# Kernel tuning notes

Measured on AMD Instinct MI355X. Metric: run time of the kernel, lower is better.

## Reference

```python
import jax, jax.numpy as jnp
import numpy as np

NUM_VIEWS = 6
NUM_HEADS = 16
NUM_LAYERS = 2
DIST_THRESHOLD = 10.0
EPS = 1e-5


def layer_norm(x, g, b):
    m = jnp.mean(x, axis=-1, keepdims=True)
    v = jnp.mean((x - m) ** 2, axis=-1, keepdims=True)
    return (x - m) / jnp.sqrt(v + EPS) * g + b


def build_mask(coords3d, num_views, threshold):
    # coords3d: (B, T, 3) -> bool mask (B, T, T), True = masked
    B, T, _ = coords3d.shape
    tpv = T // num_views
    c = jnp.nan_to_num(coords3d, nan=0.0, posinf=100.0, neginf=-100.0)
    view_ids = jnp.repeat(jnp.arange(num_views), tpv)
    same_view = view_ids[:, None] == view_ids[None, :]  # (T, T)
    dist_sq = jnp.sum((c[:, :, None, :] - c[:, None, :, :]) ** 2, axis=-1)  # (B,T,T)
    mask = same_view[None] | (dist_sq > threshold * threshold)
    all_masked = jnp.all(mask, axis=-1)  # (B, T)
    eye = jnp.eye(T, dtype=bool)
    # unmask diagonal for rows that are fully masked (matches torch fix)
    mask = jnp.where(all_masked[:, :, None] & eye[None], False, mask)
    return mask


def mha(x, qkv_w, qkv_b, out_w, out_b, mask, num_heads):
    # x: (B,T,C); qkv_w: (3C,C); out_w: (C,C); mask: (B,T,T) True=masked
    B, T, C = x.shape
    hd = C // num_heads
    qkv = x @ qkv_w.T + qkv_b  # (B,T,3C)
    q, k, v = jnp.split(qkv, 3, axis=-1)
    def heads(t):
        return t.reshape(B, T, num_heads, hd).transpose(0, 2, 1, 3)  # (B,H,T,hd)
    q, k, v = heads(q), heads(k), heads(v)
    scale = 1.0 / jnp.sqrt(jnp.asarray(hd, x.dtype))
    scores = jnp.einsum('bhqd,bhkd->bhqk', q * scale, k)
    scores = jnp.where(mask[:, None], -jnp.inf, scores)
    attn = jax.nn.softmax(scores, axis=-1)
    o = jnp.einsum('bhqk,bhkd->bhqd', attn, v)  # (B,H,T,hd)
    o = o.transpose(0, 2, 1, 3).reshape(B, T, C)
    return o @ out_w.T + out_b


def setup_inputs() -> dict:
    key = jax.random.key(0)
    B, T, C, L = 2, 1536, 1024, NUM_LAYERS
    ks = jax.random.split(key, 16)
    s = 0.02
    inp = {
        'pos_embed': jax.random.normal(ks[0], (B, T, C), jnp.float32),
        'coords3d': jax.random.normal(ks[1], (B, T, 3), jnp.float32) * 8.0,
        'ln1_g': jnp.ones((L, C), jnp.float32),
        'ln1_b': jnp.zeros((L, C), jnp.float32),
        'qkv_w': jax.random.normal(ks[2], (L, 3 * C, C), jnp.float32) * s,
        'qkv_b': jnp.zeros((L, 3 * C), jnp.float32),
        'out_w': jax.random.normal(ks[3], (L, C, C), jnp.float32) * s,
        'out_b': jnp.zeros((L, C), jnp.float32),
        'ln2_g': jnp.ones((L, C), jnp.float32),
        'ln2_b': jnp.zeros((L, C), jnp.float32),
        'ffn_w1': jax.random.normal(ks[4], (L, 4 * C, C), jnp.float32) * s,
        'ffn_b1': jnp.zeros((L, 4 * C), jnp.float32),
        'ffn_w2': jax.random.normal(ks[5], (L, C, 4 * C), jnp.float32) * s,
        'ffn_b2': jnp.zeros((L, C), jnp.float32),
        'norm_g': jnp.ones((C,), jnp.float32),
        'norm_b': jnp.zeros((C,), jnp.float32),
    }
    return inp


def reference(pos_embed, coords3d, ln1_g, ln1_b, qkv_w, qkv_b, out_w, out_b,
              ln2_g, ln2_b, ffn_w1, ffn_b1, ffn_w2, ffn_b2, norm_g, norm_b):
    mask = build_mask(coords3d, NUM_VIEWS, DIST_THRESHOLD)
    x = pos_embed
    for l in range(NUM_LAYERS):
        xn = layer_norm(x, ln1_g[l], ln1_b[l])
        x = x + mha(xn, qkv_w[l], qkv_b[l], out_w[l], out_b[l], mask, NUM_HEADS)
        xn = layer_norm(x, ln2_g[l], ln2_b[l])
        h = jax.nn.gelu(xn @ ffn_w1[l].T + ffn_b1[l], approximate=False)
        x = x + (h @ ffn_w2[l].T + ffn_b2[l])
    return layer_norm(x, norm_g, norm_b)
```

## Files before the change

### kernel.cpp

```cpp
#include <hip/hip_runtime.h>

#define TT 1536
#define CC 1024
#define NH 16
#define HD 64
#define NL 2
#define NB 2
#define MM (NB*TT)

typedef unsigned short u16;
typedef unsigned int u32;
typedef unsigned long long u64;
typedef __attribute__((ext_vector_type(8))) short short8v;
typedef __attribute__((ext_vector_type(4))) float f32x4;

__device__ __forceinline__ u16 f2bf(float f){
  u32 u = __float_as_uint(f);
  u32 r = (u + 0x7FFFu + ((u >> 16) & 1u)) >> 16;
  return (u16)r;
}

__device__ __forceinline__ void gload_lds16(const void* g, void* l){
  __builtin_amdgcn_global_load_lds(
      (const __attribute__((address_space(1))) void*)g,
      (__attribute__((address_space(3))) void*)l, 16, 0, 0);
}

__device__ __forceinline__ f32x4 mfma16(short8v a, short8v b, f32x4 c){
  return __builtin_amdgcn_mfma_f32_16x16x32_bf16(a, b, c, 0, 0, 0);
}

__device__ __forceinline__ float exp2f_fast(float x){
  return __builtin_amdgcn_exp2f(x);
}

__device__ __forceinline__ u32 cvt_pk_bf16(float lo, float hi){
  u32 r;
  asm("v_cvt_pk_bf16_f32 %0, %1, %2" : "=v"(r) : "v"(lo), "v"(hi));
  return r;
}

__device__ __forceinline__ char* ldsw(void* base, int row, int colb){
  return (char*)base + row * 128 + (colb ^ ((row & 7) << 4));
}

__global__ __launch_bounds__(256) void cvt_bf16_kernel(const float* __restrict__ in,
                                                       u16* __restrict__ out, int n4){
  int stride = gridDim.x * 256;
  for (int i = blockIdx.x * 256 + threadIdx.x; i < n4; i += stride){
    const float4 v = ((const float4*)in)[i];
    ushort4 o;
    o.x = f2bf(v.x); o.y = f2bf(v.y); o.z = f2bf(v.z); o.w = f2bf(v.w);
    ((ushort4*)out)[i] = o;
  }
}

__device__ __forceinline__ float fixc(float v){
  if (__builtin_isnan(v)) return 0.0f;
  if (__builtin_isinf(v)) return v > 0.0f ? 100.0f : -100.0f;
  return v;
}

__global__ __launch_bounds__(256) void mask_kernel(const float* __restrict__ coords,
                                                   u64* __restrict__ maskw){
  const int tid = threadIdx.x, wave = tid >> 6, lane = tid & 63;
  const int ri = blockIdx.x * 4 + wave;
  const int b = ri / TT, i = ri - b * TT;
  const float* cp = coords + (size_t)ri * 3;
  const float cx = fixc(cp[0]), cy = fixc(cp[1]), cz = fixc(cp[2]);
  const int vi = i >> 8;
  u64 allm = ~0ull;
  for (int ch = 0; ch < 24; ++ch){
    const int j = ch * 64 + lane;
    const float* cj = coords + ((size_t)b * TT + j) * 3;
    const float dx = cx - fixc(cj[0]);
    const float dy = cy - fixc(cj[1]);
    const float dz = cz - fixc(cj[2]);
    const float d2 = dx*dx + dy*dy + dz*dz;
    const bool masked = ((j >> 8) == vi) || (d2 > 100.0f);
    const u64 bal = __ballot(masked);
    if (lane == 0) maskw[(size_t)ri * 24 + ch] = bal;
    allm &= bal;
  }
  if (lane == 0 && allm == ~0ull){
    const size_t w = (size_t)ri * 24 + (i >> 6);
    maskw[w] &= ~(1ull << (i & 63));
  }
}

template<int OUTF>
__global__ __launch_bounds__(256) void ln_kernel(const float* __restrict__ x,
    const float* __restrict__ gw, const float* __restrict__ bw,
    u16* __restrict__ outb, float* __restrict__ outf){
  __shared__ float sred[4];
  const int tid = threadIdx.x, wave = tid >> 6, lane = tid & 63;
  const size_t row = blockIdx.x;
  const float4 v = *(const float4*)(x + row * CC + tid * 4);
  float s = v.x + v.y + v.z + v.w;
  #pragma unroll
  for (int o = 1; o < 64; o <<= 1) s += __shfl_xor(s, o, 64);
  if (lane == 0) sred[wave] = s;
  __syncthreads();
  const float mean = (sred[0] + sred[1] + sred[2] + sred[3]) * (1.0f / CC);
  __syncthreads();
  const float d0 = v.x - mean, d1 = v.y - mean, d2 = v.z - mean, d3 = v.w - mean;
  float q = d0*d0 + d1*d1 + d2*d2 + d3*d3;
  #pragma unroll
  for (int o = 1; o < 64; o <<= 1) q += __shfl_xor(q, o, 64);
  if (lane == 0) sred[wave] = q;
  __syncthreads();
  const float var = (sred[0] + sred[1] + sred[2] + sred[3]) * (1.0f / CC);
  const float rstd = rsqrtf(var + 1e-5f);
  const float4 g4 = *(const float4*)(gw + tid * 4);
  const float4 b4 = *(const float4*)(bw + tid * 4);
  const float y0 = d0 * rstd * g4.x + b4.x;
  const float y1 = d1 * rstd * g4.y + b4.y;
  const float y2 = d2 * rstd * g4.z + b4.z;
  const float y3 = d3 * rstd * g4.w + b4.w;
  if (OUTF){
    *(float4*)(outf + row * CC + tid * 4) = make_float4(y0, y1, y2, y3);
  } else {
    ushort4 o4; o4.x = f2bf(y0); o4.y = f2bf(y1); o4.z = f2bf(y2); o4.w = f2bf(y3);
    *(ushort4*)(outb + row * CC + tid * 4) = o4;
  }
}

template<int EPI>
__global__ __launch_bounds__(512, 4) void gemm_nt(const u16* __restrict__ A,
    const u16* __restrict__ Bw, const float* __restrict__ bias,
    u16* __restrict__ outb, float* __restrict__ outf,
    int M, int N, int K, int Ksl){
  __shared__ u16 As[2][128][64];
  __shared__ u16 Bs[2][128][64];
  const int tid = threadIdx.x, wave = tid >> 6, lane = tid & 63;
  const int gx = gridDim.x;
  const int nwg = gx * gridDim.y;
  const int orig = blockIdx.y * gx + blockIdx.x;
  const int qq = nwg >> 3, rm = nwg & 7;
  const int xcd = orig & 7, pos = orig >> 3;
  const int wg = (xcd < rm ? xcd * (qq + 1) : rm * (qq + 1) + (xcd - rm) * qq) + pos;
  const int m0 = (wg / gx) * 128, n0 = (wg % gx) * 128;
  const int kz = blockIdx.z;
  const int wr = wave >> 1, wc = wave & 1;
  f32x4 acc[2][4];
  #pragma unroll
  for (int mi = 0; mi < 2; ++mi)
    #pragma unroll
    for (int ni = 0; ni < 4; ++ni){ f32x4 z = {0.f,0.f,0.f,0.f}; acc[mi][ni] = z; }

  const u16* Ag = A + (size_t)m0 * K + (size_t)kz * Ksl;
  const u16* Bg = Bw + (size_t)n0 * K + (size_t)kz * Ksl;
  const int srow0 = wave * 8 + (lane >> 3);
  const int scole = ((lane & 7) ^ (lane >> 3)) * 8;
  auto stage = [&](int buf, int k0){
    char* ab = (char*)&As[buf][0][0];
    char* bb = (char*)&Bs[buf][0][0];
    #pragma unroll
    for (int l = 0; l < 2; ++l){
      const size_t goff = (size_t)(l*64 + srow0) * K + k0 + scole;
      const int loff = (l*8 + wave) * 1024;
      gload_lds16(Ag + goff, ab + loff);
      gload_lds16(Bg + goff, bb + loff);
    }
  };

  const int NT = Ksl >> 6;
  stage(0, 0);
  stage(1, 64);

  const int ar = lane & 15, akb = (lane >> 4) * 16;
  const int rsw = (ar & 7) << 4;
  for (int t = 0; t < NT; ++t){
    const int cur = t & 1;
    if (t + 1 < NT) asm volatile("s_waitcnt vmcnt(4)" ::: "memory");
    else            asm volatile("s_waitcnt vmcnt(0)" ::: "memory");
    __builtin_amdgcn_s_barrier();
    const char* ab = (const char*)&As[cur][0][0];
    const char* bb = (const char*)&Bs[cur][0][0];
    short8v af[2][2], bf[4][2];
    #pragma unroll
    for (int ks = 0; ks < 2; ++ks){
      const int cb = (ks*64 + akb) ^ rsw;
      #pragma unroll
      for (int mi = 0; mi < 2; ++mi)
        af[mi][ks] = *(const short8v*)(ab + (wr*32 + mi*16 + ar)*128 + cb);
      #pragma unroll
      for (int ni = 0; ni < 4; ++ni)
        bf[ni][ks] = *(const short8v*)(bb + (wc*64 + ni*16 + ar)*128 + cb);
    }
    asm volatile("s_waitcnt lgkmcnt(0)" ::: "memory");
    __builtin_amdgcn_sched_barrier(0);
    __builtin_amdgcn_s_barrier();
    if (t + 2 < NT) stage(cur, (t + 2) * 64);
    __builtin_amdgcn_s_setprio(1);
    #pragma unroll
    for (int ks = 0; ks < 2; ++ks)
      #pragma unroll
      for (int mi = 0; mi < 2; ++mi)
        #pragma unroll
        for (int ni = 0; ni < 4; ++ni)
          acc[mi][ni] = mfma16(af[mi][ks], bf[ni][ks], acc[mi][ni]);
    __builtin_amdgcn_s_setprio(0);
  }

  const int cr = (lane >> 4) * 4, cl = lane & 15;
  #pragma unroll
  for (int ni = 0; ni < 4; ++ni){
    const int c = n0 + wc*64 + ni*16 + cl;
    const float bv = bias[c];
    #pragma unroll
    for (int mi = 0; mi < 2; ++mi){
      #pragma unroll
      for (int r = 0; r < 4; ++r){
        const size_t rr2 = (size_t)(m0 + wr*32 + mi*16 + cr + r);
        float v = acc[mi][ni][r];
        if constexpr (EPI == 3){
          v += (kz == 0) ? bv : 0.0f;
          __hip_atomic_fetch_add(&outf[rr2 * N + c], v, __ATOMIC_RELAXED,
                                 __HIP_MEMORY_SCOPE_AGENT);
        } else {
          v += bv;
          if constexpr (EPI == 1) v = 0.5f * v * (1.0f + erff(v * 0.70710678118654752f));
          outb[rr2 * N + c] = f2bf(v);
        }
      }
    }
  }
}

__global__ __launch_bounds__(256, 3) void attn_kernel(const u16* __restrict__ qkv,
    const u64* __restrict__ maskw, u16* __restrict__ outp){
  __shared__ u16 Ks[2][64][64];
  __shared__ u16 Vt[2][64][64];
  __shared__ u16 Ps[4][16][64];
  const int tid = threadIdx.x, wave = tid >> 6, lane = tid & 63;
  const int b = blockIdx.y >> 4, h = blockIdx.y & 15;
  const int qb = blockIdx.x * 64;
  const int rs = 3 * CC;
  const int g4 = lane >> 4;
  const int l15 = lane & 15;
  const int qrow = qb + wave * 16 + l15;
  const u16* kv_base = qkv + (size_t)b * TT * rs;

  const float qscale = 0.18033688011112042f;
  const u16* qp = kv_base + (size_t)qrow * rs + h * HD + g4 * 8;
  short8v qf0, qf1;
  {
    const short8v r0 = *(const short8v*)qp;
    const short8v r1 = *(const short8v*)(qp + 32);
    #pragma unroll
    for (int e = 0; e < 8; ++e){
      qf0[e] = (short)f2bf(__uint_as_float(((u32)(u16)r0[e]) << 16) * qscale);
      qf1[e] = (short)f2bf(__uint_as_float(((u32)(u16)r1[e]) << 16) * qscale);
    }
  }

  f32x4 o[4], lacc;
  #pragma unroll
  for (int dt = 0; dt < 4; ++dt){ f32x4 z = {0.f,0.f,0.f,0.f}; o[dt] = z; }
  { f32x4 z = {0.f,0.f,0.f,0.f}; lacc = z; }
  float m_r = -1.0e4f;

  const int sw = (l15 & 7) << 4;
  const int swl = (lane & 7) << 4;
  int koff[4][2], voff[4][2], pwoff[4], proff[2], vwoff[2];
  #pragma unroll
  for (int jt = 0; jt < 4; ++jt){
    koff[jt][0] = (jt*16 + l15)*128 + ((g4*16) ^ sw);
    koff[jt][1] = (jt*16 + l15)*128 + ((64 + g4*16) ^ sw);
    voff[jt][0] = koff[jt][0];
    voff[jt][1] = koff[jt][1];
    pwoff[jt] = wave*2048 + l15*128 + ((jt*32 + g4*8) ^ sw);
  }
  proff[0] = wave*2048 + l15*128 + ((g4*16) ^ sw);
  proff[1] = wave*2048 + l15*128 + ((64 + g4*16) ^ sw);
  vwoff[0] = lane*128 + ((wave*16) ^ swl);
  vwoff[1] = lane*128 + ((64 + wave*16) ^ swl);

  const int scol = CC + h * HD + (((lane & 7) ^ (lane >> 3)) * 8);
  const u16* skp0 = kv_base + (size_t)(64 + wave*16 + (lane >> 3)) * rs + scol;
  const u16* skp1 = skp0 + 8 * rs;
  const u16* vp   = kv_base + (size_t)(64 + wave*8) * rs + 2*CC + h*HD + lane;
  const u64* mp2  = maskw + (size_t)(b * TT + qrow) * 24;

  char* KsB = (char*)&Ks[0][0][0];
  char* VtB = (char*)&Vt[0][0][0];
  char* PsB = (char*)&Ps[0][0][0];

  short8v vone;
  #pragma unroll
  for (int e = 0; e < 8; ++e) vone[e] = (short)0x3F80;

  {
    u16 vv[16];
    #pragma unroll
    for (int e = 0; e < 8; ++e)
      vv[e] = kv_base[(size_t)(wave*8 + e) * rs + 2*CC + h*HD + lane];
    #pragma unroll
    for (int e = 0; e < 8; ++e)
      vv[8+e] = kv_base[(size_t)(32 + wave*8 + e) * rs + 2*CC + h*HD + lane];
    gload_lds16(kv_base + (size_t)(wave*16 + (lane>>3)) * rs + scol,
                KsB + (wave*2 + 0) * 1024);
    gload_lds16(kv_base + (size_t)(wave*16 + 8 + (lane>>3)) * rs + scol,
                KsB + (wave*2 + 1) * 1024);
    short8v sv0, sv1;
    #pragma unroll
    for (int e = 0; e < 8; ++e){ sv0[e] = (short)vv[e]; sv1[e] = (short)vv[8+e]; }
    *(short8v*)(VtB + vwoff[0]) = sv0;
    *(short8v*)(VtB + vwoff[1]) = sv1;
    __syncthreads();
  }

  auto chunk = [&](int buf, bool pf){
    u16 vv[16];
    if (pf){
      #pragma unroll
      for (int e = 0; e < 8; ++e) vv[e] = vp[(size_t)e * rs];
      #pragma unroll
      for (int e = 0; e < 8; ++e) vv[8+e] = vp[(size_t)(32 + e) * rs];
      gload_lds16(skp0, KsB + (buf^1)*8192 + (wave*2 + 0)*1024);
      gload_lds16(skp1, KsB + (buf^1)*8192 + (wave*2 + 1)*1024);
    }
    const u64 mw = mp2[buf];
    const u32 mwlo = (u32)mw, mwhi = (u32)(mw >> 32);

    const char* Kb = KsB + buf * 8192;
    f32x4 S[4];
    #pragma unroll
    for (int jt = 0; jt < 4; ++jt){
      const short8v k0 = *(const short8v*)(Kb + koff[jt][0]);
      const short8v k1 = *(const short8v*)(Kb + koff[jt][1]);
      f32x4 z = {0.f,0.f,0.f,0.f};
      z = mfma16(k0, qf0, z);
      z = mfma16(k1, qf1, z);
      S[jt] = z;
    }

    float ps[16];
    float cmax = -3.0e38f;
    #pragma unroll
    for (int jt = 0; jt < 4; ++jt){
      const u32 msrc = (jt & 2) ? mwhi : mwlo;
      const int sh = g4 * 4 + (jt & 1) * 16;
      #pragma unroll
      for (int r = 0; r < 4; ++r){
        float s = S[jt][r];
        s = ((msrc >> (sh + r)) & 1u) ? -3.0e38f : s;
        ps[jt*4+r] = s;
        cmax = fmaxf(cmax, s);
      }
    }
    cmax = fmaxf(cmax, __shfl_xor(cmax, 16));
    cmax = fmaxf(cmax, __shfl_xor(cmax, 32));

    if (!__all(cmax <= m_r + 8.0f)){
      const float mnew = fmaxf(m_r, cmax);
      const float fac = exp2f_fast(m_r - mnew);
      m_r = mnew;
      float fr4[4];
      #pragma unroll
      for (int r = 0; r < 4; ++r) fr4[r] = __shfl(fac, g4 * 4 + r);
      #pragma unroll
      for (int dt = 0; dt < 4; ++dt){
        f32x4 tt = o[dt];
        tt[0] *= fr4[0]; tt[1] *= fr4[1]; tt[2] *= fr4[2]; tt[3] *= fr4[3];
        o[dt] = tt;
      }
      lacc[0] *= fr4[0]; lacc[1] *= fr4[1]; lacc[2] *= fr4[2]; lacc[3] *= fr4[3];
    }

    #pragma unroll
    for (int i = 0; i < 16; ++i) ps[i] = exp2f_fast(ps[i] - m_r);

    #pragma unroll
    for (int jt = 0; jt < 4; ++jt){
      uint2 pk;
      pk.x = cvt_pk_bf16(ps[jt*4+0], ps[jt*4+1]);
      pk.y = cvt_pk_bf16(ps[jt*4+2], ps[jt*4+3]);
      *(uint2*)(PsB + pwoff[jt]) = pk;
    }

    short8v pA[2];
    pA[0] = *(const short8v*)(PsB + proff[0]);
    pA[1] = *(const short8v*)(PsB + proff[1]);
    const char* Vb = VtB + buf * 8192;
    __builtin_amdgcn_s_setprio(1);
    #pragma unroll
    for (int dt = 0; dt < 4; ++dt){
      #pragma unroll
      for (int kc = 0; kc < 2; ++kc){
        const short8v vf = *(const short8v*)(Vb + voff[dt][kc]);
        o[dt] = mfma16(pA[kc], vf, o[dt]);
      }
    }
    lacc = mfma16(pA[0], vone, lacc);
    lacc = mfma16(pA[1], vone, lacc);
    __builtin_amdgcn_s_setprio(0);

    if (pf){
      short8v sv0, sv1;
      #pragma unroll
      for (int e = 0; e < 8; ++e){ sv0[e] = (short)vv[e]; sv1[e] = (short)vv[8+e]; }
      char* Vd = VtB + (buf^1) * 8192;
      *(short8v*)(Vd + vwoff[0]) = sv0;
      *(short8v*)(Vd + vwoff[1]) = sv1;
      vp += (size_t)64 * rs; skp0 += (size_t)64 * rs; skp1 += (size_t)64 * rs;
    }
    __syncthreads();
  };

  for (int th = 0; th < 12; ++th){
    chunk(0, true);
    chunk(1, th < 11);
    mp2 += 2;
  }

  float linv[4];
  #pragma unroll
  for (int r = 0; r < 4; ++r) linv[r] = 1.0f / fmaxf(lacc[r], 1e-30f);
  #pragma unroll
  for (int dt = 0; dt < 4; ++dt)
    #pragma unroll
    for (int r = 0; r < 4; ++r)
      outp[(size_t)(b * TT + qb + wave * 16 + g4 * 4 + r) * CC + h * HD + dt * 16 + l15] =
          f2bf(o[dt][r] * linv[r]);
}

extern "C" void kernel_launch(void* const* d_in, const int* in_sizes, int n_in,
                              void* d_out, int out_size, void* d_ws, size_t ws_size,
                              hipStream_t stream){
  (void)in_sizes; (void)n_in; (void)out_size; (void)ws_size;
  const float* pos    = (const float*)d_in[0];
  const float* coords = (const float*)d_in[1];
  const float* ln1g   = (const float*)d_in[2];
  const float* ln1b   = (const float*)d_in[3];
  const float* qkvw   = (const float*)d_in[4];
  const float* qkvbi  = (const float*)d_in[5];
  const float* outw   = (const float*)d_in[6];
  const float* outbi  = (const float*)d_in[7];
  const float* ln2g   = (const float*)d_in[8];
  const float* ln2b   = (const float*)d_in[9];
  const float* w1     = (const float*)d_in[10];
  const float* b1     = (const float*)d_in[11];
  const float* w2     = (const float*)d_in[12];
  const float* b2     = (const float*)d_in[13];
  const float* ng     = (const float*)d_in[14];
  const float* nbb    = (const float*)d_in[15];

  char* wsp = (char*)d_ws;
  size_t off = 0;
  auto alloc = [&](size_t bytes)->void*{
    void* p = wsp + off; off += (bytes + 255) & ~(size_t)255; return p;
  };
  u16* qkvw_bf = (u16*)alloc((size_t)NL*3*CC*CC*sizeof(u16));
  u16* outw_bf = (u16*)alloc((size_t)NL*CC*CC*sizeof(u16));
  u16* w1_bf   = (u16*)alloc((size_t)NL*4*CC*CC*sizeof(u16));
  u16* w2_bf   = (u16*)alloc((size_t)NL*4*CC*CC*sizeof(u16));
  float* x     = (float*)alloc((size_t)MM*CC*sizeof(float));
  u16* xn      = (u16*)alloc((size_t)MM*CC*sizeof(u16));
  u16* qkvbuf  = (u16*)alloc((size_t)MM*4*CC*sizeof(u16));
  u16* attnb   = (u16*)alloc((size_t)MM*CC*sizeof(u16));
  u64* maskw   = (u64*)alloc((size_t)MM*24*sizeof(u64));
  u16* hbuf = qkvbuf;

  auto cvt = [&](const float* s, u16* dst, size_t n){
    int n4 = (int)(n >> 2);
    int blocks = (n4 + 255) / 256; if (blocks > 4096) blocks = 4096;
    cvt_bf16_kernel<<<dim3(blocks), dim3(256), 0, stream>>>(s, dst, n4);
  };
  cvt(qkvw, qkvw_bf, (size_t)NL*3*CC*CC);
  cvt(outw, outw_bf, (size_t)NL*CC*CC);
  cvt(w1, w1_bf, (size_t)NL*4*CC*CC);
  cvt(w2, w2_bf, (size_t)NL*4*CC*CC);

  hipMemcpyAsync(x, pos, (size_t)MM*CC*sizeof(float), hipMemcpyDeviceToDevice, stream);
  mask_kernel<<<dim3(MM/4), dim3(256), 0, stream>>>(coords, maskw);

  for (int l = 0; l < NL; ++l){
    ln_kernel<0><<<dim3(MM), dim3(256), 0, stream>>>(x, ln1g + l*CC, ln1b + l*CC, xn, nullptr);
    gemm_nt<0><<<dim3(3*CC/128, MM/128, 1), dim3(512), 0, stream>>>(
        xn, qkvw_bf + (size_t)l*3*CC*CC, qkvbi + l*3*CC, qkvbuf, nullptr, MM, 3*CC, CC, CC);
    attn_kernel<<<dim3(TT/64, NB*NH), dim3(256), 0, stream>>>(qkvbuf, maskw, attnb);
    gemm_nt<3><<<dim3(CC/128, MM/128, 2), dim3(512), 0, stream>>>(
        attnb, outw_bf + (size_t)l*CC*CC, outbi + l*CC, nullptr, x, MM, CC, CC, CC/2);
    ln_kernel<0><<<dim3(MM), dim3(256), 0, stream>>>(x, ln2g + l*CC, ln2b + l*CC, xn, nullptr);
    gemm_nt<1><<<dim3(4*CC/128, MM/128, 1), dim3(512), 0, stream>>>(
        xn, w1_bf + (size_t)l*4*CC*CC, b1 + l*4*CC, hbuf, nullptr, MM, 4*CC, CC, CC);
    gemm_nt<3><<<dim3(CC/128, MM/128, 4), dim3(512), 0, stream>>>(
        hbuf, w2_bf + (size_t)l*4*CC*CC, b2 + l*CC, nullptr, x, MM, CC, 4*CC, CC);
  }
  ln_kernel<1><<<dim3(MM), dim3(256), 0, stream>>>(x, ng, nbb, nullptr, (float*)d_out);
}
```

Baseline: 489.4 us.

## Replace split-K atomic GEMMs with 64-row tiles and fused residual epilogue

The out-projection and FFN-down GEMMs no longer use split-K with float atomic adds into x. They now use a 64x128 tile variant, which doubles the number of M tiles so the grid stays reasonably large, and each output is written exactly once as bias plus residual read from x. This removes atomic traffic and the read-modify-write contention. In exchange, each workgroup runs the full K loop and the waves compute smaller fragments per tile, which may lower MFMA efficiency. The res and outf arguments alias x, but each element is read and then written by the same thread, so this is safe.

```diff
diff --git a/kernel.cpp b/kernel.cpp
--- a/kernel.cpp
+++ b/kernel.cpp
@@ -38,10 +38,6 @@
   u32 r;
   asm("v_cvt_pk_bf16_f32 %0, %1, %2" : "=v"(r) : "v"(lo), "v"(hi));
   return r;
-}
-
-__device__ __forceinline__ char* ldsw(void* base, int row, int colb){
-  return (char*)base + row * 128 + (colb ^ ((row & 7) << 4));
 }
 
 __global__ __launch_bounds__(256) void cvt_bf16_kernel(const float* __restrict__ in,
@@ -125,12 +121,12 @@
   }
 }
 
-template<int EPI>
+template<int EPI, int BM>
 __global__ __launch_bounds__(512, 4) void gemm_nt(const u16* __restrict__ A,
     const u16* __restrict__ Bw, const float* __restrict__ bias,
-    u16* __restrict__ outb, float* __restrict__ outf,
-    int M, int N, int K, int Ksl){
-  __shared__ u16 As[2][128][64];
+    const float* __restrict__ res, u16* __restrict__ outb, float* __restrict__ outf,
+    int M, int N, int K){
+  __shared__ u16 As[2][BM][64];
   __shared__ u16 Bs[2][128][64];
   const int tid = threadIdx.x, wave = tid >> 6, lane = tid & 63;
   const int gx = gridDim.x;
@@ -139,32 +135,33 @@
   const int qq = nwg >> 3, rm = nwg & 7;
   const int xcd = orig & 7, pos = orig >> 3;
   const int wg = (xcd < rm ? xcd * (qq + 1) : rm * (qq + 1) + (xcd - rm) * qq) + pos;
-  const int m0 = (wg / gx) * 128, n0 = (wg % gx) * 128;
-  const int kz = blockIdx.z;
-  const int wr = wave >> 1, wc = wave & 1;
-  f32x4 acc[2][4];
+  const int m0 = (wg / gx) * BM, n0 = (wg % gx) * 128;
+  constexpr int NFR = (BM == 128) ? 4 : 2;
+  constexpr int CW = 16 * NFR;
+  const int wr = (BM == 128) ? (wave >> 1) : (wave >> 2);
+  const int wc = (BM == 128) ? (wave & 1) : (wave & 3);
+  f32x4 acc[2][NFR];
   #pragma unroll
   for (int mi = 0; mi < 2; ++mi)
     #pragma unroll
-    for (int ni = 0; ni < 4; ++ni){ f32x4 z = {0.f,0.f,0.f,0.f}; acc[mi][ni] = z; }
-
-  const u16* Ag = A + (size_t)m0 * K + (size_t)kz * Ksl;
-  const u16* Bg = Bw + (size_t)n0 * K + (size_t)kz * Ksl;
+    for (int ni = 0; ni < NFR; ++ni){ f32x4 z = {0.f,0.f,0.f,0.f}; acc[mi][ni] = z; }
+
+  const u16* Ag = A + (size_t)m0 * K;
+  const u16* Bg = Bw + (size_t)n0 * K;
   const int srow0 = wave * 8 + (lane >> 3);
   const int scole = ((lane & 7) ^ (lane >> 3)) * 8;
   auto stage = [&](int buf, int k0){
     char* ab = (char*)&As[buf][0][0];
     char* bb = (char*)&Bs[buf][0][0];
     #pragma unroll
-    for (int l = 0; l < 2; ++l){
-      const size_t goff = (size_t)(l*64 + srow0) * K + k0 + scole;
-      const int loff = (l*8 + wave) * 1024;
-      gload_lds16(Ag + goff, ab + loff);
-      gload_lds16(Bg + goff, bb + loff);
-    }
+    for (int l = 0; l < BM/64; ++l)
+      gload_lds16(Ag + (size_t)(l*64 + srow0) * K + k0 + scole, ab + (l*8 + wave) * 1024);
+    #pragma unroll
+    for (int l = 0; l < 2; ++l)
+      gload_lds16(Bg + (size_t)(l*64 + srow0) * K + k0 + scole, bb + (l*8 + wave) * 1024);
   };
 
-  const int NT = Ksl >> 6;
+  const int NT = K >> 6;
   stage(0, 0);
   stage(1, 64);
 
@@ -172,12 +169,16 @@
   const int rsw = (ar & 7) << 4;
   for (int t = 0; t < NT; ++t){
     const int cur = t & 1;
-    if (t + 1 < NT) asm volatile("s_waitcnt vmcnt(4)" ::: "memory");
-    else            asm volatile("s_waitcnt vmcnt(0)" ::: "memory");
+    if (t + 1 < NT){
+      if constexpr (BM == 128) asm volatile("s_waitcnt vmcnt(4)" ::: "memory");
+      else                     asm volatile("s_waitcnt vmcnt(3)" ::: "memory");
+    } else {
+      asm volatile("s_waitcnt vmcnt(0)" ::: "memory");
+    }
     __builtin_amdgcn_s_barrier();
     const char* ab = (const char*)&As[cur][0][0];
     const char* bb = (const char*)&Bs[cur][0][0];
-    short8v af[2][2], bf[4][2];
+    short8v af[2][2], bf[NFR][2];
     #pragma unroll
     for (int ks = 0; ks < 2; ++ks){
       const int cb = (ks*64 + akb) ^ rsw;
@@ -185,8 +186,8 @@
       for (int mi = 0; mi < 2; ++mi)
         af[mi][ks] = *(const short8v*)(ab + (wr*32 + mi*16 + ar)*128 + cb);
       #pragma unroll
-      for (int ni = 0; ni < 4; ++ni)
-        bf[ni][ks] = *(const short8v*)(bb + (wc*64 + ni*16 + ar)*128 + cb);
+      for (int ni = 0; ni < NFR; ++ni)
+        bf[ni][ks] = *(const short8v*)(bb + (wc*CW + ni*16 + ar)*128 + cb);
     }
     asm volatile("s_waitcnt lgkmcnt(0)" ::: "memory");
     __builtin_amdgcn_sched_barrier(0);
@@ -198,31 +199,25 @@
       #pragma unroll
       for (int mi = 0; mi < 2; ++mi)
         #pragma unroll
-        for (int ni = 0; ni < 4; ++ni)
+        for (int ni = 0; ni < NFR; ++ni)
           acc[mi][ni] = mfma16(af[mi][ks], bf[ni][ks], acc[mi][ni]);
     __builtin_amdgcn_s_setprio(0);
   }
 
   const int cr = (lane >> 4) * 4, cl = lane & 15;
   #pragma unroll
-  for (int ni = 0; ni < 4; ++ni){
-    const int c = n0 + wc*64 + ni*16 + cl;
+  for (int ni = 0; ni < NFR; ++ni){
+    const int c = n0 + wc*CW + ni*16 + cl;
     const float bv = bias[c];
     #pragma unroll
     for (int mi = 0; mi < 2; ++mi){
       #pragma unroll
       for (int r = 0; r < 4; ++r){
         const size_t rr2 = (size_t)(m0 + wr*32 + mi*16 + cr + r);
-        float v = acc[mi][ni][r];
-        if constexpr (EPI == 3){
-          v += (kz == 0) ? bv : 0.0f;
-          __hip_atomic_fetch_add(&outf[rr2 * N + c], v, __ATOMIC_RELAXED,
-                                 __HIP_MEMORY_SCOPE_AGENT);
-        } else {
-          v += bv;
-          if constexpr (EPI == 1) v = 0.5f * v * (1.0f + erff(v * 0.70710678118654752f));
-          outb[rr2 * N + c] = f2bf(v);
-        }
+        float v = acc[mi][ni][r] + bv;
+        if constexpr (EPI == 1) v = 0.5f * v * (1.0f + erff(v * 0.70710678118654752f));
+        if constexpr (EPI == 2) outf[rr2 * N + c] = v + res[rr2 * N + c];
+        else outb[rr2 * N + c] = f2bf(v);
       }
     }
   }
@@ -478,16 +473,16 @@
 
   for (int l = 0; l < NL; ++l){
     ln_kernel<0><<<dim3(MM), dim3(256), 0, stream>>>(x, ln1g + l*CC, ln1b + l*CC, xn, nullptr);
-    gemm_nt<0><<<dim3(3*CC/128, MM/128, 1), dim3(512), 0, stream>>>(
-        xn, qkvw_bf + (size_t)l*3*CC*CC, qkvbi + l*3*CC, qkvbuf, nullptr, MM, 3*CC, CC, CC);
+    gemm_nt<0,128><<<dim3(3*CC/128, MM/128), dim3(512), 0, stream>>>(
+        xn, qkvw_bf + (size_t)l*3*CC*CC, qkvbi + l*3*CC, nullptr, qkvbuf, nullptr, MM, 3*CC, CC);
     attn_kernel<<<dim3(TT/64, NB*NH), dim3(256), 0, stream>>>(qkvbuf, maskw, attnb);
-    gemm_nt<3><<<dim3(CC/128, MM/128, 2), dim3(512), 0, stream>>>(
-        attnb, outw_bf + (size_t)l*CC*CC, outbi + l*CC, nullptr, x, MM, CC, CC, CC/2);
+    gemm_nt<2,64><<<dim3(CC/128, MM/64), dim3(512), 0, stream>>>(
+        attnb, outw_bf + (size_t)l*CC*CC, outbi + l*CC, x, nullptr, x, MM, CC, CC);
     ln_kernel<0><<<dim3(MM), dim3(256), 0, stream>>>(x, ln2g + l*CC, ln2b + l*CC, xn, nullptr);
-    gemm_nt<1><<<dim3(4*CC/128, MM/128, 1), dim3(512), 0, stream>>>(
-        xn, w1_bf + (size_t)l*4*CC*CC, b1 + l*4*CC, hbuf, nullptr, MM, 4*CC, CC, CC);
-    gemm_nt<3><<<dim3(CC/128, MM/128, 4), dim3(512), 0, stream>>>(
-        hbuf, w2_bf + (size_t)l*4*CC*CC, b2 + l*CC, nullptr, x, MM, CC, 4*CC, CC);
+    gemm_nt<1,128><<<dim3(4*CC/128, MM/128), dim3(512), 0, stream>>>(
+        xn, w1_bf + (size_t)l*4*CC*CC, b1 + l*4*CC, nullptr, hbuf, nullptr, MM, 4*CC, CC);
+    gemm_nt<2,64><<<dim3(CC/128, MM/64), dim3(512), 0, stream>>>(
+        hbuf, w2_bf + (size_t)l*4*CC*CC, b2 + l*CC, x, nullptr, x, MM, CC, 4*CC);
   }
   ln_kernel<1><<<dim3(MM), dim3(256), 0, stream>>>(x, ng, nbb, nullptr, (float*)d_out);
 }
```

Measured after the change: 432.4 us. 1.13x faster.
